# Performance work log

Measured on AMD Instinct MI355X. Metric: run time of the kernel, lower is better.

Reference implementation:

```python
import jax, jax.numpy as jnp
import numpy as np

EPS = 1e-08

def _householder(x, v):
    # x: [B,S,r], v: [B,S,r]; H x = x - 2 v_n (v_n . x), v_n = v/||v||
    v_norm_sq = jnp.sum(v * v, axis=-1, keepdims=True) + EPS
    v_n = v / jnp.sqrt(v_norm_sq)
    vTx = jnp.sum(x * v_n, axis=-1, keepdims=True)
    return x - 2.0 * v_n * vTx

def setup_inputs() -> dict:
    key = jax.random.key(0)
    ks = jax.random.split(key, 8)
    B, S, D, R = 4, 4096, 1024, 256
    N_IN, N_PROC, N_OUT, K = 16, 64, 16, 8
    x = jax.random.normal(ks[0], (B, S, D), dtype=jnp.float32)
    input_idx = jax.random.randint(ks[1], (B, S), 0, N_IN)
    process_indices = jax.random.randint(ks[2], (B, S, K), 0, N_PROC)
    output_idx = jax.random.randint(ks[3], (B, S), 0, N_OUT)
    # learned params (orthogonal-ish init approximated by scaled gaussian)
    input_neurons = jax.random.normal(ks[4], (N_IN, D, R), dtype=jnp.float32) / np.sqrt(D)
    pv = jax.random.normal(ks[5], (N_PROC, R), dtype=jnp.float32)
    process_neurons = pv / (jnp.linalg.norm(pv, axis=-1, keepdims=True) + EPS)
    output_neurons = jax.random.normal(ks[6], (N_OUT, R, D), dtype=jnp.float32) / np.sqrt(D)
    return {"x": x, "input_neurons": input_neurons, "process_neurons": process_neurons,
            "output_neurons": output_neurons, "input_idx": input_idx,
            "process_indices": process_indices, "output_idx": output_idx}

def reference(x, input_neurons, process_neurons, output_neurons,
              input_idx, process_indices, output_idx):
    # ---- input projection (hard selection): d_model -> rank ----
    # compute all-expert projections then gather per token (avoids [B,S,D,R] gather)
    all_in = jnp.einsum('bsd,ndr->bsnr', x, input_neurons)          # [B,S,n_in,R]
    h = jnp.take_along_axis(all_in, input_idx[..., None, None], axis=2)[:, :, 0, :]  # [B,S,R]
    # ---- process: k sequential Householder reflections ----
    selected_v = process_neurons[process_indices]                    # [B,S,k,R]
    vs = jnp.moveaxis(selected_v, 2, 0)                              # [k,B,S,R]
    def step(carry, v):
        return _householder(carry, v), None
    h, _ = jax.lax.scan(step, h, vs)
    # ---- output projection (hard selection): rank -> d_model ----
    all_out = jnp.einsum('bsr,nrd->bsnd', h, output_neurons)         # [B,S,n_out,D]
    out = jnp.take_along_axis(all_out, output_idx[..., None, None], axis=2)[:, :, 0, :]
    return out
```

## Files before the change

kernel.cpp:

```cpp
#include <hip/hip_runtime.h>
#include <hip/hip_bf16.h>

#define NT    16384
#define DM    1024
#define RK    256
#define N_IN  16
#define N_OUT 16
#define KHH   8
#define MAXTOK 1536
#define BM    64
#define TPE   (MAXTOK / BM)
#define KC    4
#define IN_BLKS  (8 * TPE * 8)
#define OUT_BLKS (8 * TPE * 16)
#define TWOUT_BLKS (16 * 64)
#define CVT_BLKS  2048

typedef short bf16x8 __attribute__((ext_vector_type(8)));
typedef float f32x4 __attribute__((ext_vector_type(4)));
typedef unsigned short u16;
typedef u16 u16x8 __attribute__((ext_vector_type(8)));
typedef u16 u16x4 __attribute__((ext_vector_type(4)));

__device__ __forceinline__ u16 f2bf(float f) {
  __hip_bfloat16 b = __float2bfloat16(f);
  return *reinterpret_cast<u16*>(&b);
}
__device__ __forceinline__ float bf2f(u16 u) {
  return __uint_as_float((unsigned)u << 16);
}

__device__ __forceinline__ void gl_lds16(const void* g, void* lds) {
  __builtin_amdgcn_global_load_lds(
      (const __attribute__((address_space(1))) void*)g,
      (__attribute__((address_space(3))) void*)lds, 16, 0, 0);
}

__device__ __forceinline__ void transpose_tile(
    const float* __restrict__ src, u16* __restrict__ dst,
    int R, int C, int e, int tile, float (*ls)[65], int t) {
  const int tilesC = C >> 6;
  const int tr = (tile / tilesC) << 6;
  const int tc = (tile % tilesC) << 6;
  const int row = t >> 2, q = t & 3;
  const float* s = src + (size_t)e * R * C + (size_t)(tr + row) * C + tc + q * 16;
#pragma unroll
  for (int j = 0; j < 4; j++) {
    const float4 v = ((const float4*)s)[j];
    ls[row][q * 16 + j * 4 + 0] = v.x;
    ls[row][q * 16 + j * 4 + 1] = v.y;
    ls[row][q * 16 + j * 4 + 2] = v.z;
    ls[row][q * 16 + j * 4 + 3] = v.w;
  }
  __syncthreads();
  const int cc = t >> 2;
  u16x8 o0, o1;
#pragma unroll
  for (int j = 0; j < 8; j++) o0[j] = f2bf(ls[q * 16 + j][cc]);
#pragma unroll
  for (int j = 0; j < 8; j++) o1[j] = f2bf(ls[q * 16 + 8 + j][cc]);
  u16* d = dst + (size_t)e * C * R + (size_t)(tc + cc) * R + tr + q * 16;
  ((u16x8*)d)[0] = o0;
  ((u16x8*)d)[1] = o1;
}

__global__ __launch_bounds__(256) void lists_pn_winT_cvt(
    const int* __restrict__ in_idx, const int* __restrict__ out_idx,
    const float* __restrict__ pn, const float* __restrict__ Win,
    const float* __restrict__ x,
    int* __restrict__ list_in, int* __restrict__ cnt_in,
    int* __restrict__ list_out, int* __restrict__ cnt_out,
    float* __restrict__ pnorm2, u16* __restrict__ WinT,
    u16* __restrict__ xb) {
  const int b = blockIdx.x;
  const int tid = threadIdx.x, lane = tid & 63, wid = tid >> 6;
  __shared__ float ls[64][65];
  __shared__ int wsum[4];

  if (b >= 33 + 1024) {
    const int bc = b - (33 + 1024);
#pragma unroll
    for (int g = 0; g < 4; ++g) {
      const size_t i = (size_t)bc * 256 + tid + (size_t)g * (CVT_BLKS * 256);
      const float4 a = ((const float4*)x)[2 * i];
      const float4 c = ((const float4*)x)[2 * i + 1];
      u16x8 o;
      o[0] = f2bf(a.x); o[1] = f2bf(a.y); o[2] = f2bf(a.z); o[3] = f2bf(a.w);
      o[4] = f2bf(c.x); o[5] = f2bf(c.y); o[6] = f2bf(c.z); o[7] = f2bf(c.w);
      ((u16x8*)xb)[i] = o;
    }
    return;
  }
  if (b >= 33) {
    const int b2 = b - 33;
    const int e = b2 >> 6, tile = b2 & 63;
    const int tilesC = RK >> 6;
    const int tr = (tile / tilesC) << 6;
    const int tc = (tile % tilesC) << 6;
    const int row = tid >> 2, q = tid & 3;
    const float* s = Win + (size_t)e * DM * RK + (size_t)(tr + row) * RK + tc + q * 16;
#pragma unroll
    for (int j = 0; j < 4; j++) {
      const float4 v = ((const float4*)s)[j];
      ls[row][q * 16 + j * 4 + 0] = v.x;
      ls[row][q * 16 + j * 4 + 1] = v.y;
      ls[row][q * 16 + j * 4 + 2] = v.z;
      ls[row][q * 16 + j * 4 + 3] = v.w;
    }
    __syncthreads();
    const int cc = tid >> 2;
    u16x8 o0, o1;
#pragma unroll
    for (int j = 0; j < 8; j++) o0[j] = f2bf(ls[q * 16 + j][cc]);
#pragma unroll
    for (int j = 0; j < 8; j++) o1[j] = f2bf(ls[q * 16 + 8 + j][cc]);
    const int D = tr + q * 16;
    const int kc = D >> 8, dk = D & 255;
    u16* d = WinT + ((size_t)(e * KC + kc) * RK + (tc + cc)) * 256 + dk;
    ((u16x8*)d)[0] = o0;
    ((u16x8*)d)[1] = o1;
    return;
  }
  if (b == 32) {
    const int p = tid >> 2, q = tid & 3;
    const float* row = pn + (size_t)p * RK + q * 64;
    float s = 0.f;
#pragma unroll
    for (int i = 0; i < 16; i++) {
      const float4 v = ((const float4*)row)[i];
      s += v.x * v.x + v.y * v.y + v.z * v.z + v.w * v.w;
    }
    s += __shfl_xor(s, 1);
    s += __shfl_xor(s, 2);
    if (q == 0) pnorm2[p] = s + 1e-8f;
    return;
  }

  const int e = b & 15, which = b >> 4;
  const int* __restrict__ idx = which ? out_idx : in_idx;
  int* __restrict__ list = (which ? list_out : list_in) + (size_t)e * NT;
  int* __restrict__ cnt = (which ? cnt_out : cnt_in) + e;

  const unsigned long long lt = (1ull << lane) - 1ull;
  int off = 0;
  for (int base = 0; base < NT; base += 1024) {
    const int4 iv = ((const int4*)(idx + base))[tid];
    const bool f0 = iv.x == e, f1 = iv.y == e, f2 = iv.z == e, f3 = iv.w == e;
    const unsigned long long m0 = __ballot(f0), m1 = __ballot(f1),
                             m2 = __ballot(f2), m3 = __ballot(f3);
    const int below = __popcll(m0 & lt) + __popcll(m1 & lt) +
                      __popcll(m2 & lt) + __popcll(m3 & lt);
    const int wtot = __popcll(m0) + __popcll(m1) + __popcll(m2) + __popcll(m3);
    if (lane == 0) wsum[wid] = wtot;
    __syncthreads();
    int b0 = 0, tot = 0;
#pragma unroll
    for (int w = 0; w < 4; w++) { if (w < wid) b0 += wsum[w]; tot += wsum[w]; }
    int pos = off + b0 + below;
    const int t = base + tid * 4;
    if (f0) list[pos++] = t;
    if (f1) list[pos++] = t + 1;
    if (f2) list[pos++] = t + 2;
    if (f3) list[pos++] = t + 3;
    off += tot;
    __syncthreads();
  }
  if (tid == 0) *cnt = off;
}

__global__ __launch_bounds__(256, 3) void input_gemm_woT(
    const u16* __restrict__ xb, const u16* __restrict__ WinT,
    const int* __restrict__ list, const int* __restrict__ cnt,
    u16* __restrict__ h4,
    const float* __restrict__ Wout, u16* __restrict__ WoT) {
  __shared__ __align__(16) char smem[41216];
  const int tid = threadIdx.x, lane = tid & 63, w = tid >> 6;
  const int bid = blockIdx.x;

  if (bid >= IN_BLKS) {
    const int b2 = bid - IN_BLKS;
    transpose_tile(Wout, WoT, RK, DM, b2 >> 6, b2 & 63,
                   (float(*)[65])smem, tid);
    return;
  }

  const int xcd = bid & 7;
  int j = bid >> 3;
  const int tile = j % TPE;
  j /= TPE;
  const int e = xcd * 2 + (j & 1);
  const int kc = j >> 1;
  const int nt = cnt[e];
  const int t0 = tile * BM;
  if (t0 >= nt) return;
  const int* __restrict__ lst = list + (size_t)e * NT + t0;
  const int ntok = min(BM, nt - t0);

  u16* As = (u16*)smem;
  u16* Bs = (u16*)(smem + 8192);
  int* toks = (int*)(smem + 8192 + 32768);

  if (tid < BM) toks[tid] = lst[tid < ntok ? tid : 0];
  __syncthreads();

  const int sub = lane >> 3;
  const int swz8 = ((lane & 7) ^ sub) * 8;
  const u16* Wbase = WinT + (size_t)(e * KC + kc) * RK * 256;
  const int ar0 = (w * 2 + 0) * 8 + sub;
  const int ar1 = (w * 2 + 1) * 8 + sub;
  const u16* asrc0 = xb + (size_t)toks[ar0] * DM + kc * 256 + swz8;
  const u16* asrc1 = xb + (size_t)toks[ar1] * DM + kc * 256 + swz8;

  f32x4 acc[4][4];
#pragma unroll
  for (int m = 0; m < 4; m++)
#pragma unroll
    for (int jx = 0; jx < 4; jx++) acc[m][jx] = (f32x4)0.f;

  const int l15 = lane & 15, lg = lane >> 4;

#pragma unroll
  for (int it = 0; it < 4; ++it) {
    const int k0 = it * 64;
    if (it) __syncthreads();
    gl_lds16(asrc0 + k0, As + (w * 2 + 0) * 512);
    gl_lds16(asrc1 + k0, As + (w * 2 + 1) * 512);
#pragma unroll
    for (int i = 0; i < 8; ++i) {
      const int g = w * 8 + i;
      const int n = g * 8 + sub;
      gl_lds16(Wbase + (size_t)n * 256 + k0 + swz8, Bs + g * 512);
    }
    __syncthreads();
#pragma unroll
    for (int kk = 0; kk < 2; ++kk) {
      const int sw = (((kk * 4 + lg) ^ (l15 & 7)) << 4);
      bf16x8 fa[4];
#pragma unroll
      for (int m = 0; m < 4; ++m)
        fa[m] = *(const bf16x8*)((const char*)As + (m * 16 + l15) * 128 + sw);
#pragma unroll
      for (int jx = 0; jx < 4; ++jx) {
        const int n = w * 64 + jx * 16 + l15;
        const bf16x8 fb = *(const bf16x8*)((const char*)Bs + n * 128 + sw);
#pragma unroll
        for (int m = 0; m < 4; ++m)
          acc[m][jx] = __builtin_amdgcn_mfma_f32_16x16x32_bf16(fa[m], fb, acc[m][jx], 0, 0, 0);
      }
    }
  }

  u16* hp4 = h4 + (size_t)kc * NT * RK;
#pragma unroll
  for (int m = 0; m < 4; ++m)
#pragma unroll
    for (int r = 0; r < 4; ++r) {
      const int slot = m * 16 + lg * 4 + r;
      if (slot < ntok) {
        u16* hp = hp4 + (size_t)toks[slot] * RK + w * 64 + l15;
#pragma unroll
        for (int jx = 0; jx < 4; ++jx) hp[jx * 16] = f2bf(acc[m][jx][r]);
      }
    }
}

__global__ __launch_bounds__(256) void hh_k(
    const u16* __restrict__ h4, u16* __restrict__ hb,
    const float* __restrict__ pn, const float* __restrict__ pnorm2,
    const int* __restrict__ pidx) {
  const int lane = threadIdx.x & 63;
  const int t = blockIdx.x * 4 + (threadIdx.x >> 6);

  float4 hv;
  {
    const u16x4 p0 = ((const u16x4*)(h4 + ((size_t)0 * NT + t) * RK))[lane];
    const u16x4 p1 = ((const u16x4*)(h4 + ((size_t)1 * NT + t) * RK))[lane];
    const u16x4 p2 = ((const u16x4*)(h4 + ((size_t)2 * NT + t) * RK))[lane];
    const u16x4 p3 = ((const u16x4*)(h4 + ((size_t)3 * NT + t) * RK))[lane];
    hv.x = (bf2f(p0[0]) + bf2f(p1[0])) + (bf2f(p2[0]) + bf2f(p3[0]));
    hv.y = (bf2f(p0[1]) + bf2f(p1[1])) + (bf2f(p2[1]) + bf2f(p3[1]));
    hv.z = (bf2f(p0[2]) + bf2f(p1[2])) + (bf2f(p2[2]) + bf2f(p3[2]));
    hv.w = (bf2f(p0[3]) + bf2f(p1[3])) + (bf2f(p2[3]) + bf2f(p3[3]));
  }

#pragma unroll
  for (int k = 0; k < KHH; k++) {
    const int p = pidx[t * KHH + k];
    const float4 v = ((const float4*)(pn + (size_t)p * RK))[lane];
    float dvh = v.x * hv.x + v.y * hv.y + v.z * hv.z + v.w * hv.w;
#pragma unroll
    for (int s = 32; s; s >>= 1) dvh += __shfl_xor(dvh, s);
    const float c = 2.f * dvh / pnorm2[p];
    hv.x = fmaf(-c, v.x, hv.x);
    hv.y = fmaf(-c, v.y, hv.y);
    hv.z = fmaf(-c, v.z, hv.z);
    hv.w = fmaf(-c, v.w, hv.w);
  }
  u16x4 o;
  o[0] = f2bf(hv.x); o[1] = f2bf(hv.y); o[2] = f2bf(hv.z); o[3] = f2bf(hv.w);
  ((u16x4*)(hb + (size_t)t * RK))[lane] = o;
}

__global__ __launch_bounds__(256, 6) void output_gemm_mfma(
    const u16* __restrict__ hb, const u16* __restrict__ WoT,
    const int* __restrict__ list, const int* __restrict__ cnt,
    float* __restrict__ out) {
  const int bid = blockIdx.x;
  const int xcd = bid & 7;
  int j = bid >> 3;
  const int tile = j % TPE;
  j /= TPE;
  const int e = xcd * 2 + (j & 1);
  const int cb = j >> 1;
  const int nt = cnt[e];
  const int t0 = tile * BM;
  if (t0 >= nt) return;
  const int* __restrict__ lst = list + (size_t)e * NT + t0;
  const int ntok = min(BM, nt - t0);

  __shared__ __align__(16) u16 As[BM * 64];
  __shared__ __align__(16) u16 Bs[128 * 64];
  __shared__ int toks[BM];

  const int tid = threadIdx.x, lane = tid & 63, w = tid >> 6;
  if (tid < BM) toks[tid] = lst[tid < ntok ? tid : 0];
  __syncthreads();

  const int sub = lane >> 3;
  const int swz8 = ((lane & 7) ^ sub) * 8;
  const u16* Wbase = WoT + (size_t)e * DM * RK + (size_t)(cb * 128) * RK;
  const int ar0 = (w * 2 + 0) * 8 + sub;
  const int ar1 = (w * 2 + 1) * 8 + sub;
  const u16* asrc0 = hb + (size_t)toks[ar0] * RK + swz8;
  const u16* asrc1 = hb + (size_t)toks[ar1] * RK + swz8;

  f32x4 acc[4][2];
#pragma unroll
  for (int m = 0; m < 4; m++)
#pragma unroll
    for (int jx = 0; jx < 2; jx++) acc[m][jx] = (f32x4)0.f;

  const int l15 = lane & 15, lg = lane >> 4;

#pragma unroll
  for (int it = 0; it < RK / 64; ++it) {
    const int k0 = it * 64;
    if (it) __syncthreads();
    gl_lds16(asrc0 + k0, As + (w * 2 + 0) * 512);
    gl_lds16(asrc1 + k0, As + (w * 2 + 1) * 512);
#pragma unroll
    for (int i = 0; i < 4; ++i) {
      const int g = w * 4 + i;
      const int n = g * 8 + sub;
      gl_lds16(Wbase + (size_t)n * RK + k0 + swz8, Bs + g * 512);
    }
    __syncthreads();
#pragma unroll
    for (int kk = 0; kk < 2; ++kk) {
      const int sw = (((kk * 4 + lg) ^ (l15 & 7)) << 4);
      bf16x8 fa[4];
#pragma unroll
      for (int m = 0; m < 4; ++m)
        fa[m] = *(const bf16x8*)((const char*)As + (m * 16 + l15) * 128 + sw);
#pragma unroll
      for (int jx = 0; jx < 2; ++jx) {
        const int n = w * 32 + jx * 16 + l15;
        const bf16x8 fb = *(const bf16x8*)((const char*)Bs + n * 128 + sw);
#pragma unroll
        for (int m = 0; m < 4; ++m)
          acc[m][jx] = __builtin_amdgcn_mfma_f32_16x16x32_bf16(fa[m], fb, acc[m][jx], 0, 0, 0);
      }
    }
  }

#pragma unroll
  for (int m = 0; m < 4; ++m)
#pragma unroll
    for (int r = 0; r < 4; ++r) {
      const int slot = m * 16 + lg * 4 + r;
      if (slot < ntok) {
        float* op = out + (size_t)toks[slot] * DM + cb * 128 + w * 32 + l15;
#pragma unroll
        for (int jx = 0; jx < 2; ++jx) op[jx * 16] = acc[m][jx][r];
      }
    }
}

extern "C" void kernel_launch(void* const* d_in, const int* in_sizes, int n_in,
                              void* d_out, int out_size, void* d_ws,
                              size_t ws_size, hipStream_t stream) {
  const float* x     = (const float*)d_in[0];
  const float* Win   = (const float*)d_in[1];
  const float* pn    = (const float*)d_in[2];
  const float* Wout  = (const float*)d_in[3];
  const int* in_idx  = (const int*)d_in[4];
  const int* pidx    = (const int*)d_in[5];
  const int* out_idx = (const int*)d_in[6];
  float* out = (float*)d_out;

  char* ws = (char*)d_ws;
  u16* WinT  = (u16*)ws;                    ws += (size_t)N_IN * RK * DM * 2;
  u16* WoT   = (u16*)ws;                    ws += (size_t)N_OUT * DM * RK * 2;
  u16* hb    = (u16*)ws;                    ws += (size_t)NT * RK * 2;
  u16* h4    = (u16*)ws;                    ws += (size_t)KC * NT * RK * 2;
  u16* xb    = (u16*)ws;                    ws += (size_t)NT * DM * 2;
  int* list_in  = (int*)ws;                 ws += (size_t)N_IN * NT * 4;
  int* list_out = (int*)ws;                 ws += (size_t)N_OUT * NT * 4;
  int* cnt_in   = (int*)ws;                 ws += 64;
  int* cnt_out  = (int*)ws;                 ws += 64;
  float* pnorm2 = (float*)ws;

  hipLaunchKernelGGL(lists_pn_winT_cvt, dim3(33 + 1024 + CVT_BLKS), dim3(256),
                     0, stream, in_idx, out_idx, pn, Win, x, list_in, cnt_in,
                     list_out, cnt_out, pnorm2, WinT, xb);
  hipLaunchKernelGGL(input_gemm_woT, dim3(IN_BLKS + TWOUT_BLKS), dim3(256),
                     0, stream, xb, WinT, list_in, cnt_in, h4, Wout, WoT);
  hipLaunchKernelGGL(hh_k, dim3(NT / 4), dim3(256), 0, stream,
                     h4, hb, pn, pnorm2, pidx);
  hipLaunchKernelGGL(output_gemm_mfma, dim3(OUT_BLKS), dim3(256), 0, stream,
                     hb, WoT, list_out, cnt_out, out);
}
```

Measured before the change: 86.69 us.

## Fuse fp32-to-bf16 conversion of x into input GEMM A-tile loading

Removes the separate pass that converts all of x to bf16 in a workspace buffer. The input GEMM now reads fp32 x rows directly into registers, prefetching all four k-steps up front, then converts them to bf16 and stores them to swizzled LDS in place of the async global-to-LDS load. This drops one full write and read of the bf16 copy of x. In exchange, each A tile now reads twice as many bytes, and the prefetch adds register pressure and VALU conversion work inside the GEMM.

```diff
diff --git a/kernel.cpp b/kernel.cpp
--- a/kernel.cpp
+++ b/kernel.cpp
@@ -14,7 +14,6 @@
 #define IN_BLKS  (8 * TPE * 8)
 #define OUT_BLKS (8 * TPE * 16)
 #define TWOUT_BLKS (16 * 64)
-#define CVT_BLKS  2048
 
 typedef short bf16x8 __attribute__((ext_vector_type(8)));
 typedef float f32x4 __attribute__((ext_vector_type(4)));
@@ -64,33 +63,17 @@
   ((u16x8*)d)[1] = o1;
 }
 
-__global__ __launch_bounds__(256) void lists_pn_winT_cvt(
+__global__ __launch_bounds__(256) void lists_pn_winT(
     const int* __restrict__ in_idx, const int* __restrict__ out_idx,
     const float* __restrict__ pn, const float* __restrict__ Win,
-    const float* __restrict__ x,
     int* __restrict__ list_in, int* __restrict__ cnt_in,
     int* __restrict__ list_out, int* __restrict__ cnt_out,
-    float* __restrict__ pnorm2, u16* __restrict__ WinT,
-    u16* __restrict__ xb) {
+    float* __restrict__ pnorm2, u16* __restrict__ WinT) {
   const int b = blockIdx.x;
   const int tid = threadIdx.x, lane = tid & 63, wid = tid >> 6;
   __shared__ float ls[64][65];
   __shared__ int wsum[4];
 
-  if (b >= 33 + 1024) {
-    const int bc = b - (33 + 1024);
-#pragma unroll
-    for (int g = 0; g < 4; ++g) {
-      const size_t i = (size_t)bc * 256 + tid + (size_t)g * (CVT_BLKS * 256);
-      const float4 a = ((const float4*)x)[2 * i];
-      const float4 c = ((const float4*)x)[2 * i + 1];
-      u16x8 o;
-      o[0] = f2bf(a.x); o[1] = f2bf(a.y); o[2] = f2bf(a.z); o[3] = f2bf(a.w);
-      o[4] = f2bf(c.x); o[5] = f2bf(c.y); o[6] = f2bf(c.z); o[7] = f2bf(c.w);
-      ((u16x8*)xb)[i] = o;
-    }
-    return;
-  }
   if (b >= 33) {
     const int b2 = b - 33;
     const int e = b2 >> 6, tile = b2 & 63;
@@ -169,7 +152,7 @@
 }
 
 __global__ __launch_bounds__(256, 3) void input_gemm_woT(
-    const u16* __restrict__ xb, const u16* __restrict__ WinT,
+    const float* __restrict__ x, const u16* __restrict__ WinT,
     const int* __restrict__ list, const int* __restrict__ cnt,
     u16* __restrict__ h4,
     const float* __restrict__ Wout, u16* __restrict__ WoT) {
@@ -203,13 +186,15 @@
   if (tid < BM) toks[tid] = lst[tid < ntok ? tid : 0];
   __syncthreads();
 
+  const int arow = tid >> 3, k8 = tid & 7;
+  const float* axp0 = x + (size_t)toks[arow] * DM + kc * 256 + k8 * 8;
+  const float* axp1 = x + (size_t)toks[arow + 32] * DM + kc * 256 + k8 * 8;
+  const int aoff0 = arow * 128 + ((k8 ^ (arow & 7)) << 4);
+  const int aoff1 = (arow + 32) * 128 + ((k8 ^ (arow & 7)) << 4);
+
   const int sub = lane >> 3;
   const int swz8 = ((lane & 7) ^ sub) * 8;
   const u16* Wbase = WinT + (size_t)(e * KC + kc) * RK * 256;
-  const int ar0 = (w * 2 + 0) * 8 + sub;
-  const int ar1 = (w * 2 + 1) * 8 + sub;
-  const u16* asrc0 = xb + (size_t)toks[ar0] * DM + kc * 256 + swz8;
-  const u16* asrc1 = xb + (size_t)toks[ar1] * DM + kc * 256 + swz8;
 
   f32x4 acc[4][4];
 #pragma unroll
@@ -218,19 +203,37 @@
     for (int jx = 0; jx < 4; jx++) acc[m][jx] = (f32x4)0.f;
 
   const int l15 = lane & 15, lg = lane >> 4;
+
+  float4 af[4][2][2];
+#pragma unroll
+  for (int p = 0; p < 4; ++p) {
+    af[p][0][0] = ((const float4*)(axp0 + p * 64))[0];
+    af[p][0][1] = ((const float4*)(axp0 + p * 64))[1];
+    af[p][1][0] = ((const float4*)(axp1 + p * 64))[0];
+    af[p][1][1] = ((const float4*)(axp1 + p * 64))[1];
+  }
 
 #pragma unroll
   for (int it = 0; it < 4; ++it) {
     const int k0 = it * 64;
     if (it) __syncthreads();
-    gl_lds16(asrc0 + k0, As + (w * 2 + 0) * 512);
-    gl_lds16(asrc1 + k0, As + (w * 2 + 1) * 512);
+    u16x8 a0, a1;
+    a0[0] = f2bf(af[it][0][0].x); a0[1] = f2bf(af[it][0][0].y);
+    a0[2] = f2bf(af[it][0][0].z); a0[3] = f2bf(af[it][0][0].w);
+    a0[4] = f2bf(af[it][0][1].x); a0[5] = f2bf(af[it][0][1].y);
+    a0[6] = f2bf(af[it][0][1].z); a0[7] = f2bf(af[it][0][1].w);
+    a1[0] = f2bf(af[it][1][0].x); a1[1] = f2bf(af[it][1][0].y);
+    a1[2] = f2bf(af[it][1][0].z); a1[3] = f2bf(af[it][1][0].w);
+    a1[4] = f2bf(af[it][1][1].x); a1[5] = f2bf(af[it][1][1].y);
+    a1[6] = f2bf(af[it][1][1].z); a1[7] = f2bf(af[it][1][1].w);
 #pragma unroll
     for (int i = 0; i < 8; ++i) {
       const int g = w * 8 + i;
       const int n = g * 8 + sub;
       gl_lds16(Wbase + (size_t)n * 256 + k0 + swz8, Bs + g * 512);
     }
+    *(u16x8*)((char*)As + aoff0) = a0;
+    *(u16x8*)((char*)As + aoff1) = a1;
     __syncthreads();
 #pragma unroll
     for (int kk = 0; kk < 2; ++kk) {
@@ -403,18 +406,17 @@
   u16* WoT   = (u16*)ws;                    ws += (size_t)N_OUT * DM * RK * 2;
   u16* hb    = (u16*)ws;                    ws += (size_t)NT * RK * 2;
   u16* h4    = (u16*)ws;                    ws += (size_t)KC * NT * RK * 2;
-  u16* xb    = (u16*)ws;                    ws += (size_t)NT * DM * 2;
   int* list_in  = (int*)ws;                 ws += (size_t)N_IN * NT * 4;
   int* list_out = (int*)ws;                 ws += (size_t)N_OUT * NT * 4;
   int* cnt_in   = (int*)ws;                 ws += 64;
   int* cnt_out  = (int*)ws;                 ws += 64;
   float* pnorm2 = (float*)ws;
 
-  hipLaunchKernelGGL(lists_pn_winT_cvt, dim3(33 + 1024 + CVT_BLKS), dim3(256),
-                     0, stream, in_idx, out_idx, pn, Win, x, list_in, cnt_in,
-                     list_out, cnt_out, pnorm2, WinT, xb);
+  hipLaunchKernelGGL(lists_pn_winT, dim3(33 + 1024), dim3(256), 0, stream,
+                     in_idx, out_idx, pn, Win, list_in, cnt_in,
+                     list_out, cnt_out, pnorm2, WinT);
   hipLaunchKernelGGL(input_gemm_woT, dim3(IN_BLKS + TWOUT_BLKS), dim3(256),
-                     0, stream, xb, WinT, list_in, cnt_in, h4, Wout, WoT);
+                     0, stream, x, WinT, list_in, cnt_in, h4, Wout, WoT);
   hipLaunchKernelGGL(hh_k, dim3(NT / 4), dim3(256), 0, stream,
                      h4, hb, pn, pnorm2, pidx);
   hipLaunchKernelGGL(output_gemm_mfma, dim3(OUT_BLKS), dim3(256), 0, stream,
```

After: 80.80 us. 6.8% less time.
